# Performance work log

Measured on AMD Instinct MI355X. Metric: run time of the kernel, lower is better.

Reference implementation:

```python
import jax, jax.numpy as jnp
import numpy as np

B, C, H, W = 32, 1024, 32, 32
KC, VC = 1024, 1024  # key_channels must equal H*W; value_channels must equal in_channels


def setup_inputs() -> dict:
    key = jax.random.key(0)
    ks = jax.random.split(key, 8)
    s = 1.0 / np.sqrt(C)
    return {
        "x": jax.random.normal(ks[0], (B, C, H, W), dtype=jnp.float32),
        "Wq": jax.random.normal(ks[1], (KC, C), dtype=jnp.float32) * s,
        "bq": jax.random.normal(ks[2], (KC,), dtype=jnp.float32) * 0.01,
        "Wk": jax.random.normal(ks[3], (KC, C), dtype=jnp.float32) * s,
        "bk": jax.random.normal(ks[4], (KC,), dtype=jnp.float32) * 0.01,
        "Wv": jax.random.normal(ks[5], (VC, C), dtype=jnp.float32) * s,
        "bv": jax.random.normal(ks[6], (VC,), dtype=jnp.float32) * 0.01,
        # torch init is zeros(1); use a nonzero scalar so the attention path is exercised
        "gamma": jax.random.normal(ks[7], (1,), dtype=jnp.float32) * 0.5,
    }


def reference(x, Wq, bq, Wk, bk, Wv, bv, gamma):
    b, c, h, w = x.shape
    n = h * w
    xf = x.reshape(b, c, n)  # [B, C, N]
    # 1x1 convs == per-position channel projections
    q = jnp.einsum('kc,bcn->bkn', Wq, xf) + bq[None, :, None]  # [B, Kc, N]
    k = jnp.einsum('kc,bcn->bkn', Wk, xf) + bk[None, :, None]  # [B, Kc, N]
    v = jnp.einsum('vc,bcn->bvn', Wv, xf) + bv[None, :, None]  # [B, Cv, N]
    # bmm(query, key^T): contracts spatial dim -> channel-channel attention [B, Kc, Kc]
    attn = jax.nn.softmax(jnp.einsum('bin,bjn->bij', q, k), axis=-1)
    # bmm(value, attention): value's spatial dim (== Kc) contracts with attn rows
    out = jnp.einsum('bvn,bnk->bvk', v, attn)  # [B, Cv, Kc] with Kc == N
    out = out.reshape(b, -1, h, w)
    return gamma * out + x
```

## Files before the change

kernel.cpp:

```cpp
#include <hip/hip_runtime.h>
#include <cstdint>

typedef __fp16 f16x8 __attribute__((ext_vector_type(8)));
typedef __fp16 f16x4 __attribute__((ext_vector_type(4)));
typedef float  f32x4 __attribute__((ext_vector_type(4)));

static constexpr int NDIM = 1024;

static constexpr long long OFF_W     = 0;
static constexpr long long OFF_BIAS  = 6291456;
static constexpr long long OFF_XT    = 6303744;
static constexpr long long OFF_S     = 0;
static constexpr long long OFF_QKV   = 134217728;
static constexpr long long OFF_STATS = OFF_QKV + 2097152;

__device__ __forceinline__ void async16(__fp16* lds, const __fp16* g) {
  __builtin_amdgcn_global_load_lds(
      (const __attribute__((address_space(1))) void*)g,
      (__attribute__((address_space(3))) void*)lds, 16, 0, 0);
}

__global__ __launch_bounds__(256) void cast_w(const float* __restrict__ Wq,
                                              const float* __restrict__ Wk,
                                              const float* __restrict__ Wv,
                                              __fp16* __restrict__ W3) {
  const int i = blockIdx.x * 256 + threadIdx.x;
  const int which = i >> 18;
  const int j = i & 262143;
  const float* src = which == 0 ? Wq : (which == 1 ? Wk : Wv);
  const float4 v = ((const float4*)src)[j];
  f16x4 o = {(__fp16)v.x, (__fp16)v.y, (__fp16)v.z, (__fp16)v.w};
  ((f16x4*)W3)[i] = o;
}

__global__ __launch_bounds__(256) void pack_bias(const float* __restrict__ bq,
                                                 const float* __restrict__ bk,
                                                 const float* __restrict__ bv,
                                                 float* __restrict__ b3) {
  const int i = blockIdx.x * 256 + threadIdx.x;
  if (i < 1024) b3[i] = bq[i];
  else if (i < 2048) b3[i] = bk[i - 1024];
  else if (i < 3072) b3[i] = bv[i - 2048];
}

__global__ __launch_bounds__(256) void transpose_cast_x(const float* __restrict__ x,
                                                        __fp16* __restrict__ xT) {
  __shared__ float t[32][33];
  const int b = blockIdx.z;
  const int n0 = blockIdx.x * 32, c0 = blockIdx.y * 32;
  const float* xb = x + (long long)b * NDIM * NDIM;
  __fp16* ob = xT + (long long)b * NDIM * NDIM;
  const int tx = threadIdx.x & 31, ty = threadIdx.x >> 5;
#pragma unroll
  for (int i = ty; i < 32; i += 8)
    t[i][tx] = xb[(long long)(c0 + i) * NDIM + n0 + tx];
  __syncthreads();
#pragma unroll
  for (int i = ty; i < 32; i += 8)
    ob[(long long)(n0 + i) * NDIM + c0 + tx] = (__fp16)t[tx][i];
}


#define STAGE_A(NXT, KN)                                                            \
  async16(&As[(NXT)*8192 + tid*8],        A  + (long long)(m0 + sRow)       * 1024 + (KN) + sCol); \
  async16(&As[(NXT)*8192 + 4096 + tid*8], A  + (long long)(m0 + 128 + sRow) * 1024 + (KN) + sCol);

#define STAGE_B(NXT, KN)                                                            \
  async16(&Bs[(NXT)*8192 + tid*8],        Bp + (long long)(n0 + sRow)       * 1024 + (KN) + sCol); \
  async16(&Bs[(NXT)*8192 + 4096 + tid*8], Bp + (long long)(n0 + 128 + sRow) * 1024 + (KN) + sCol);

#define TILE(BUF, NXT, KN)                                                          \
  asm volatile("s_waitcnt vmcnt(8)" ::: "memory");                                  \
  __builtin_amdgcn_s_barrier();                                                     \
  STAGE_A(NXT, KN)                                                                  \
  STAGE_B(NXT, KN)                                                                  \
  bf[0] = *(const f16x8*)&Bs[(BUF)*8192 + bBase + 0*512];                           \
  bf[1] = *(const f16x8*)&Bs[(BUF)*8192 + bBase + 1*512];                           \
  _Pragma("unroll")                                                                 \
  for (int mf = 0; mf < 8; ++mf)                                                    \
    af[mf] = *(const f16x8*)&As[(BUF)*8192 + aBase + mf*512];                       \
  bf[2] = *(const f16x8*)&Bs[(BUF)*8192 + bBase + 2*512];                           \
  bf[3] = *(const f16x8*)&Bs[(BUF)*8192 + bBase + 3*512];                           \
  _Pragma("unroll")                                                                 \
  for (int mf = 0; mf < 8; ++mf) {                                                  \
    _Pragma("unroll")                                                               \
    for (int nf = 0; nf < 4; ++nf)                                                  \
      acc[mf][nf] = __builtin_amdgcn_mfma_f32_16x16x32_f16(af[mf], bf[nf], acc[mf][nf], 0, 0, 0); \
  }

template <int EPI>
__global__ __launch_bounds__(512, 2)
void gemm256(const __fp16* __restrict__ Ag, const __fp16* __restrict__ Bg,
             void* __restrict__ Cout, const float* __restrict__ bias,
             const float* __restrict__ X, const float* __restrict__ gamma,
             long long sA, long long sB, long long sC) {
  __shared__ alignas(16) __fp16 As[4 * 8192];
  __shared__ alignas(16) __fp16 Bs[4 * 8192];

  const int tid  = threadIdx.x;
  const int wid  = tid >> 6, lane = tid & 63;
  const int wm   = wid >> 2, wn = wid & 3;
  const int g    = lane >> 4, r = lane & 15;
  const int b    = blockIdx.z;
  const int m0   = blockIdx.y * 256;
  const int n0   = blockIdx.x * 256;

  const __fp16* A  = Ag + (long long)b * sA;
  const __fp16* Bp = Bg + (long long)b * sB;

  const int sRow = tid >> 2;
  const int sCol = ((tid & 3) ^ ((tid >> 3) & 3)) * 8;

  const int fcol  = (g ^ ((r >> 1) & 3)) * 8;
  const int aBase = (wm * 128 + r) * 32 + fcol;
  const int bBase = (wn * 64 + r) * 32 + fcol;

  f16x8 af[8];
  f16x8 bf[4];
  f32x4 acc[8][4];
#pragma unroll
  for (int i = 0; i < 8; ++i)
#pragma unroll
    for (int j = 0; j < 4; ++j) acc[i][j] = f32x4{0.f, 0.f, 0.f, 0.f};

  STAGE_A(0, 0)  STAGE_B(0, 0)
  STAGE_A(1, 32) STAGE_B(1, 32)
  STAGE_A(2, 64) STAGE_B(2, 64)

  for (int t0 = 0; t0 < 1024; t0 += 128) {
    const int ka  = t0 + 96;
    const int k0n = (ka < 1024) ? ka : 0;
    const int k1n = (ka + 32 < 1024) ? ka + 32 : 0;
    const int k2n = (ka + 64 < 1024) ? ka + 64 : 0;
    const int k3n = (ka + 96 < 1024) ? ka + 96 : 0;
    TILE(0, 3, k0n)
    TILE(1, 0, k1n)
    TILE(2, 1, k2n)
    TILE(3, 2, k3n)
  }

  const float g2 = (EPI == 2) ? gamma[0] : 0.f;
  const int ccol  = n0 + wn * 64 + r;
  const int crow0 = m0 + wm * 128 + g * 4;
#pragma unroll
  for (int mf = 0; mf < 8; ++mf) {
#pragma unroll
    for (int reg = 0; reg < 4; ++reg) {
      const int row = crow0 + mf * 16 + reg;
      const long long rb = (long long)b * sC + (long long)row * 1024;
      const float bb = (EPI == 0) ? bias[row] : 0.f;
#pragma unroll
      for (int nf = 0; nf < 4; ++nf) {
        const int col = ccol + nf * 16;
        const float v = acc[mf][nf][reg];
        if (EPI == 0)      ((__fp16*)Cout)[rb + col] = (__fp16)(v + bb);
        else if (EPI == 1) ((float*)Cout)[rb + col] = v;
        else               ((float*)Cout)[rb + col] = g2 * v + X[rb + col];
      }
    }
  }
}

__global__ __launch_bounds__(256) void row_stats(const float* __restrict__ S,
                                                 float2* __restrict__ stats) {
  const int row = blockIdx.x * 4 + (threadIdx.x >> 6);
  const int lane = threadIdx.x & 63;
  const float4* rp = (const float4*)(S + (long long)row * NDIM);
  float4 v[4];
  float m = -3.4e38f;
#pragma unroll
  for (int j = 0; j < 4; j++) {
    v[j] = rp[lane + 64 * j];
    m = fmaxf(m, fmaxf(fmaxf(v[j].x, v[j].y), fmaxf(v[j].z, v[j].w)));
  }
#pragma unroll
  for (int o = 32; o; o >>= 1) m = fmaxf(m, __shfl_xor(m, o));
  float s = 0.f;
#pragma unroll
  for (int j = 0; j < 4; j++)
    s += __expf(v[j].x - m) + __expf(v[j].y - m) + __expf(v[j].z - m) + __expf(v[j].w - m);
#pragma unroll
  for (int o = 32; o; o >>= 1) s += __shfl_xor(s, o);
  if (lane == 0) stats[row] = make_float2(m, 1.f / s);
}

__global__ __launch_bounds__(256) void softmax_transpose(const float* __restrict__ S,
                                                         const float2* __restrict__ stats,
                                                         __fp16* __restrict__ attnT) {
  __shared__ __fp16 t[64][72];
  const int b = blockIdx.z;
  const int i0 = blockIdx.y * 64, j0 = blockIdx.x * 64;
  const float* Sb = S + (long long)b * NDIM * NDIM;
  const float2* st = stats + b * NDIM;
  const int tr = threadIdx.x >> 4;
  const int tc = (threadIdx.x & 15) * 4;
#pragma unroll
  for (int it = 0; it < 4; it++) {
    const int i = tr + 16 * it;
    const float4 vv = *(const float4*)&Sb[(long long)(i0 + i) * NDIM + j0 + tc];
    const float2 ms = st[i0 + i];
    t[tc + 0][i] = (__fp16)(__expf(vv.x - ms.x) * ms.y);
    t[tc + 1][i] = (__fp16)(__expf(vv.y - ms.x) * ms.y);
    t[tc + 2][i] = (__fp16)(__expf(vv.z - ms.x) * ms.y);
    t[tc + 3][i] = (__fp16)(__expf(vv.w - ms.x) * ms.y);
  }
  __syncthreads();
  __fp16* Ab = attnT + (long long)b * 3145728;
#pragma unroll
  for (int it = 0; it < 4; it++) {
    const int j = tr + 16 * it;
    f16x4 o = {t[j][tc], t[j][tc + 1], t[j][tc + 2], t[j][tc + 3]};
    *(f16x4*)&Ab[(long long)(j0 + j) * NDIM + i0 + tc] = o;
  }
}

extern "C" void kernel_launch(void* const* d_in, const int* in_sizes, int n_in,
                              void* d_out, int out_size, void* d_ws, size_t ws_size,
                              hipStream_t stream) {
  const float* x     = (const float*)d_in[0];
  const float* Wq    = (const float*)d_in[1];
  const float* bq    = (const float*)d_in[2];
  const float* Wk    = (const float*)d_in[3];
  const float* bk    = (const float*)d_in[4];
  const float* Wv    = (const float*)d_in[5];
  const float* bv    = (const float*)d_in[6];
  const float* gamma = (const float*)d_in[7];
  char* ws = (char*)d_ws;

  __fp16* W3    = (__fp16*)(ws + OFF_W);
  float*  bias3 = (float*)(ws + OFF_BIAS);
  __fp16* xT    = (__fp16*)(ws + OFF_XT);
  float*  S     = (float*)(ws + OFF_S);
  __fp16* QKV   = (__fp16*)(ws + OFF_QKV);
  float2* stats = (float2*)(ws + OFF_STATS);
  float*  out   = (float*)d_out;

  cast_w<<<3072, 256, 0, stream>>>(Wq, Wk, Wv, W3);
  pack_bias<<<12, 256, 0, stream>>>(bq, bk, bv, bias3);
  transpose_cast_x<<<dim3(32, 32, 32), 256, 0, stream>>>(x, xT);

  gemm256<0><<<dim3(4, 12, 32), 512, 0, stream>>>(
      W3, xT, QKV, bias3, nullptr, nullptr,
      0LL, 1048576LL, 3145728LL);

  gemm256<1><<<dim3(4, 4, 32), 512, 0, stream>>>(
      QKV, QKV + 1048576, S, nullptr, nullptr, nullptr,
      3145728LL, 3145728LL, 1048576LL);

  row_stats<<<8192, 256, 0, stream>>>(S, stats);
  softmax_transpose<<<dim3(16, 16, 32), 256, 0, stream>>>(S, stats, QKV);

  gemm256<2><<<dim3(4, 4, 32), 512, 0, stream>>>(
      QKV + 2097152, QKV, out, nullptr, x, gamma,
      3145728LL, 3145728LL, 1048576LL);
}
```

Measured before the change: 532.0 us.

## Fuse softmax row statistics into the QK GEMM epilogue and compute S transposed

The QK GEMM now computes S transposed (K·Qᵀ), so softmax rows become columns. Its epilogue reduces per-column partial max and sum-exp through LDS and writes them to a scratch buffer held in the output tensor. A small finalize kernel merges the four partials, and an elementwise kernel applies exp and normalisation with coalesced reads and writes. This replaces the separate row_stats pass over S and the LDS-transposing softmax kernel, and it also merges the weight-cast and bias-pack launches. The cost is extra epilogue work and reductions inside the GEMM, plus reuse of the output buffer as scratch before the final GEMM overwrites it.

```diff
diff --git a/kernel.cpp b/kernel.cpp
--- a/kernel.cpp
+++ b/kernel.cpp
@@ -12,7 +12,6 @@
 static constexpr long long OFF_XT    = 6303744;
 static constexpr long long OFF_S     = 0;
 static constexpr long long OFF_QKV   = 134217728;
-static constexpr long long OFF_STATS = OFF_QKV + 2097152;
 
 __device__ __forceinline__ void async16(__fp16* lds, const __fp16* g) {
   __builtin_amdgcn_global_load_lds(
@@ -20,27 +19,26 @@
       (__attribute__((address_space(3))) void*)lds, 16, 0, 0);
 }
 
-__global__ __launch_bounds__(256) void cast_w(const float* __restrict__ Wq,
+__global__ __launch_bounds__(256) void prep_w(const float* __restrict__ Wq,
                                               const float* __restrict__ Wk,
                                               const float* __restrict__ Wv,
-                                              __fp16* __restrict__ W3) {
-  const int i = blockIdx.x * 256 + threadIdx.x;
-  const int which = i >> 18;
-  const int j = i & 262143;
-  const float* src = which == 0 ? Wq : (which == 1 ? Wk : Wv);
-  const float4 v = ((const float4*)src)[j];
-  f16x4 o = {(__fp16)v.x, (__fp16)v.y, (__fp16)v.z, (__fp16)v.w};
-  ((f16x4*)W3)[i] = o;
-}
-
-__global__ __launch_bounds__(256) void pack_bias(const float* __restrict__ bq,
-                                                 const float* __restrict__ bk,
-                                                 const float* __restrict__ bv,
-                                                 float* __restrict__ b3) {
-  const int i = blockIdx.x * 256 + threadIdx.x;
-  if (i < 1024) b3[i] = bq[i];
-  else if (i < 2048) b3[i] = bk[i - 1024];
-  else if (i < 3072) b3[i] = bv[i - 2048];
+                                              const float* __restrict__ bq,
+                                              const float* __restrict__ bk,
+                                              const float* __restrict__ bv,
+                                              __fp16* __restrict__ W3,
+                                              float* __restrict__ b3) {
+  if (blockIdx.x < 3072) {
+    const int i = blockIdx.x * 256 + threadIdx.x;
+    const int which = i >> 18;
+    const int j = i & 262143;
+    const float* src = which == 0 ? Wq : (which == 1 ? Wk : Wv);
+    const float4 v = ((const float4*)src)[j];
+    f16x4 o = {(__fp16)v.x, (__fp16)v.y, (__fp16)v.z, (__fp16)v.w};
+    ((f16x4*)W3)[i] = o;
+  } else {
+    for (int k = threadIdx.x; k < 3072; k += 256)
+      b3[k] = (k < 1024) ? bq[k] : (k < 2048) ? bk[k - 1024] : bv[k - 2048];
+  }
 }
 
 __global__ __launch_bounds__(256) void transpose_cast_x(const float* __restrict__ x,
@@ -93,6 +91,7 @@
 void gemm256(const __fp16* __restrict__ Ag, const __fp16* __restrict__ Bg,
              void* __restrict__ Cout, const float* __restrict__ bias,
              const float* __restrict__ X, const float* __restrict__ gamma,
+             float2* __restrict__ part,
              long long sA, long long sB, long long sC) {
   __shared__ alignas(16) __fp16 As[4 * 8192];
   __shared__ alignas(16) __fp16 Bs[4 * 8192];
@@ -142,6 +141,39 @@
   const float g2 = (EPI == 2) ? gamma[0] : 0.f;
   const int ccol  = n0 + wn * 64 + r;
   const int crow0 = m0 + wm * 128 + g * 4;
+
+  if (EPI == 1) {
+    asm volatile("s_waitcnt vmcnt(0)" ::: "memory");
+    __syncthreads();
+    float2* LDSp = (float2*)As;
+#pragma unroll
+    for (int nf = 0; nf < 4; ++nf) {
+      float pm = -3.4e38f;
+#pragma unroll
+      for (int mf = 0; mf < 8; ++mf)
+#pragma unroll
+        for (int rg = 0; rg < 4; ++rg) pm = fmaxf(pm, acc[mf][nf][rg]);
+      pm = fmaxf(pm, __shfl_xor(pm, 16));
+      pm = fmaxf(pm, __shfl_xor(pm, 32));
+      float ps = 0.f;
+#pragma unroll
+      for (int mf = 0; mf < 8; ++mf)
+#pragma unroll
+        for (int rg = 0; rg < 4; ++rg) ps += __expf(acc[mf][nf][rg] - pm);
+      ps += __shfl_xor(ps, 16);
+      ps += __shfl_xor(ps, 32);
+      if (lane < 16)
+        LDSp[(wn * 64 + nf * 16 + r) * 2 + wm] = make_float2(pm, ps);
+    }
+    __syncthreads();
+    if (tid < 256) {
+      const float2 a = LDSp[tid * 2 + 0], c2 = LDSp[tid * 2 + 1];
+      const float M = fmaxf(a.x, c2.x);
+      const float Sv = a.y * __expf(a.x - M) + c2.y * __expf(c2.x - M);
+      part[(long long)blockIdx.y * 32768 + b * 1024 + n0 + tid] = make_float2(M, Sv);
+    }
+  }
+
 #pragma unroll
   for (int mf = 0; mf < 8; ++mf) {
 #pragma unroll
@@ -161,56 +193,45 @@
   }
 }
 
-__global__ __launch_bounds__(256) void row_stats(const float* __restrict__ S,
-                                                 float2* __restrict__ stats) {
-  const int row = blockIdx.x * 4 + (threadIdx.x >> 6);
-  const int lane = threadIdx.x & 63;
-  const float4* rp = (const float4*)(S + (long long)row * NDIM);
-  float4 v[4];
-  float m = -3.4e38f;
-#pragma unroll
-  for (int j = 0; j < 4; j++) {
-    v[j] = rp[lane + 64 * j];
-    m = fmaxf(m, fmaxf(fmaxf(v[j].x, v[j].y), fmaxf(v[j].z, v[j].w)));
-  }
-#pragma unroll
-  for (int o = 32; o; o >>= 1) m = fmaxf(m, __shfl_xor(m, o));
-  float s = 0.f;
-#pragma unroll
-  for (int j = 0; j < 4; j++)
-    s += __expf(v[j].x - m) + __expf(v[j].y - m) + __expf(v[j].z - m) + __expf(v[j].w - m);
-#pragma unroll
-  for (int o = 32; o; o >>= 1) s += __shfl_xor(s, o);
-  if (lane == 0) stats[row] = make_float2(m, 1.f / s);
-}
-
-__global__ __launch_bounds__(256) void softmax_transpose(const float* __restrict__ S,
-                                                         const float2* __restrict__ stats,
-                                                         __fp16* __restrict__ attnT) {
-  __shared__ __fp16 t[64][72];
-  const int b = blockIdx.z;
-  const int i0 = blockIdx.y * 64, j0 = blockIdx.x * 64;
-  const float* Sb = S + (long long)b * NDIM * NDIM;
-  const float2* st = stats + b * NDIM;
-  const int tr = threadIdx.x >> 4;
-  const int tc = (threadIdx.x & 15) * 4;
-#pragma unroll
-  for (int it = 0; it < 4; it++) {
-    const int i = tr + 16 * it;
-    const float4 vv = *(const float4*)&Sb[(long long)(i0 + i) * NDIM + j0 + tc];
-    const float2 ms = st[i0 + i];
-    t[tc + 0][i] = (__fp16)(__expf(vv.x - ms.x) * ms.y);
-    t[tc + 1][i] = (__fp16)(__expf(vv.y - ms.x) * ms.y);
-    t[tc + 2][i] = (__fp16)(__expf(vv.z - ms.x) * ms.y);
-    t[tc + 3][i] = (__fp16)(__expf(vv.w - ms.x) * ms.y);
-  }
-  __syncthreads();
-  __fp16* Ab = attnT + (long long)b * 3145728;
-#pragma unroll
-  for (int it = 0; it < 4; it++) {
-    const int j = tr + 16 * it;
-    f16x4 o = {t[j][tc], t[j][tc + 1], t[j][tc + 2], t[j][tc + 3]};
-    *(f16x4*)&Ab[(long long)(j0 + j) * NDIM + i0 + tc] = o;
+__global__ __launch_bounds__(256) void finalize_stats(const float2* __restrict__ part,
+                                                      float2* __restrict__ stats) {
+  const int i = blockIdx.x * 256 + threadIdx.x;
+  float2 p0 = part[i];
+  float2 p1 = part[32768 + i];
+  float2 p2 = part[65536 + i];
+  float2 p3 = part[98304 + i];
+  float M = fmaxf(fmaxf(p0.x, p1.x), fmaxf(p2.x, p3.x));
+  float S = p0.y * __expf(p0.x - M) + p1.y * __expf(p1.x - M) +
+            p2.y * __expf(p2.x - M) + p3.y * __expf(p3.x - M);
+  stats[i] = make_float2(M, 1.f / S);
+}
+
+__global__ __launch_bounds__(256) void softmax_elem(const float* __restrict__ St,
+                                                    const float2* __restrict__ stats,
+                                                    __fp16* __restrict__ attnT) {
+  const long long idx0 = ((long long)blockIdx.x * 256 + threadIdx.x) * 16;
+  const int b   = (int)(idx0 >> 20);
+  const int rem = (int)(idx0 & 1048575);
+  const int n0  = rem & 1023;
+  const float4* src = (const float4*)(St + idx0);
+  const float2* st  = stats + b * 1024 + n0;
+  __fp16* dst = attnT + (long long)b * 3145728 + rem;
+  float w[16];
+#pragma unroll
+  for (int j = 0; j < 4; ++j) {
+    const float4 v = src[j];
+    const float2 s0 = st[j * 4 + 0], s1 = st[j * 4 + 1], s2 = st[j * 4 + 2], s3 = st[j * 4 + 3];
+    w[j * 4 + 0] = __expf(v.x - s0.x) * s0.y;
+    w[j * 4 + 1] = __expf(v.y - s1.x) * s1.y;
+    w[j * 4 + 2] = __expf(v.z - s2.x) * s2.y;
+    w[j * 4 + 3] = __expf(v.w - s3.x) * s3.y;
+  }
+#pragma unroll
+  for (int h = 0; h < 2; ++h) {
+    f16x8 o;
+#pragma unroll
+    for (int e = 0; e < 8; ++e) o[e] = (__fp16)w[h * 8 + e];
+    *(f16x8*)(dst + h * 8) = o;
   }
 }
 
@@ -230,27 +251,27 @@
   __fp16* W3    = (__fp16*)(ws + OFF_W);
   float*  bias3 = (float*)(ws + OFF_BIAS);
   __fp16* xT    = (__fp16*)(ws + OFF_XT);
-  float*  S     = (float*)(ws + OFF_S);
+  float*  St    = (float*)(ws + OFF_S);
   __fp16* QKV   = (__fp16*)(ws + OFF_QKV);
-  float2* stats = (float2*)(ws + OFF_STATS);
   float*  out   = (float*)d_out;
-
-  cast_w<<<3072, 256, 0, stream>>>(Wq, Wk, Wv, W3);
-  pack_bias<<<12, 256, 0, stream>>>(bq, bk, bv, bias3);
+  float2* part  = (float2*)d_out;
+  float2* stats = (float2*)d_out + 131072;
+
+  prep_w<<<3073, 256, 0, stream>>>(Wq, Wk, Wv, bq, bk, bv, W3, bias3);
   transpose_cast_x<<<dim3(32, 32, 32), 256, 0, stream>>>(x, xT);
 
   gemm256<0><<<dim3(4, 12, 32), 512, 0, stream>>>(
-      W3, xT, QKV, bias3, nullptr, nullptr,
+      W3, xT, QKV, bias3, nullptr, nullptr, nullptr,
       0LL, 1048576LL, 3145728LL);
 
   gemm256<1><<<dim3(4, 4, 32), 512, 0, stream>>>(
-      QKV, QKV + 1048576, S, nullptr, nullptr, nullptr,
+      QKV + 1048576, QKV, St, nullptr, nullptr, nullptr, part,
       3145728LL, 3145728LL, 1048576LL);
 
-  row_stats<<<8192, 256, 0, stream>>>(S, stats);
-  softmax_transpose<<<dim3(16, 16, 32), 256, 0, stream>>>(S, stats, QKV);
+  finalize_stats<<<128, 256, 0, stream>>>(part, stats);
+  softmax_elem<<<8192, 256, 0, stream>>>(St, stats, QKV);
 
   gemm256<2><<<dim3(4, 4, 32), 512, 0, stream>>>(
-      QKV + 2097152, QKV, out, nullptr, x, gamma,
+      QKV + 2097152, QKV, out, nullptr, x, gamma, nullptr,
       3145728LL, 3145728LL, 1048576LL);
 }
```

After: 544.8 us. 2.4% more time.

## Fuse softmax row statistics into QK^T GEMM epilogue and merge prep kernels

Applied to the files above, without the earlier changes.

The QK^T GEMM epilogue now computes per-row partial max and sum-of-exp over each 256-column tile. It reduces them across waves through LDS and writes the partials to a scratch area inside the output buffer. A small finalize kernel merges the four partials per row, replacing the row_stats kernel that re-read the whole 128MB score matrix. The weight cast and bias pack are also merged into one launch. This trades a full pass over S for extra epilogue work and reuses the output buffer as temporary storage, which the final GEMM later overwrites.

```diff
diff --git a/kernel.cpp b/kernel.cpp
--- a/kernel.cpp
+++ b/kernel.cpp
@@ -12,7 +12,6 @@
 static constexpr long long OFF_XT    = 6303744;
 static constexpr long long OFF_S     = 0;
 static constexpr long long OFF_QKV   = 134217728;
-static constexpr long long OFF_STATS = OFF_QKV + 2097152;
 
 __device__ __forceinline__ void async16(__fp16* lds, const __fp16* g) {
   __builtin_amdgcn_global_load_lds(
@@ -20,27 +19,26 @@
       (__attribute__((address_space(3))) void*)lds, 16, 0, 0);
 }
 
-__global__ __launch_bounds__(256) void cast_w(const float* __restrict__ Wq,
+__global__ __launch_bounds__(256) void prep_w(const float* __restrict__ Wq,
                                               const float* __restrict__ Wk,
                                               const float* __restrict__ Wv,
-                                              __fp16* __restrict__ W3) {
-  const int i = blockIdx.x * 256 + threadIdx.x;
-  const int which = i >> 18;
-  const int j = i & 262143;
-  const float* src = which == 0 ? Wq : (which == 1 ? Wk : Wv);
-  const float4 v = ((const float4*)src)[j];
-  f16x4 o = {(__fp16)v.x, (__fp16)v.y, (__fp16)v.z, (__fp16)v.w};
-  ((f16x4*)W3)[i] = o;
-}
-
-__global__ __launch_bounds__(256) void pack_bias(const float* __restrict__ bq,
-                                                 const float* __restrict__ bk,
-                                                 const float* __restrict__ bv,
-                                                 float* __restrict__ b3) {
-  const int i = blockIdx.x * 256 + threadIdx.x;
-  if (i < 1024) b3[i] = bq[i];
-  else if (i < 2048) b3[i] = bk[i - 1024];
-  else if (i < 3072) b3[i] = bv[i - 2048];
+                                              const float* __restrict__ bq,
+                                              const float* __restrict__ bk,
+                                              const float* __restrict__ bv,
+                                              __fp16* __restrict__ W3,
+                                              float* __restrict__ b3) {
+  if (blockIdx.x < 3072) {
+    const int i = blockIdx.x * 256 + threadIdx.x;
+    const int which = i >> 18;
+    const int j = i & 262143;
+    const float* src = which == 0 ? Wq : (which == 1 ? Wk : Wv);
+    const float4 v = ((const float4*)src)[j];
+    f16x4 o = {(__fp16)v.x, (__fp16)v.y, (__fp16)v.z, (__fp16)v.w};
+    ((f16x4*)W3)[i] = o;
+  } else {
+    for (int k = threadIdx.x; k < 3072; k += 256)
+      b3[k] = (k < 1024) ? bq[k] : (k < 2048) ? bk[k - 1024] : bv[k - 2048];
+  }
 }
 
 __global__ __launch_bounds__(256) void transpose_cast_x(const float* __restrict__ x,
@@ -93,6 +91,7 @@
 void gemm256(const __fp16* __restrict__ Ag, const __fp16* __restrict__ Bg,
              void* __restrict__ Cout, const float* __restrict__ bias,
              const float* __restrict__ X, const float* __restrict__ gamma,
+             float2* __restrict__ part,
              long long sA, long long sB, long long sC) {
   __shared__ alignas(16) __fp16 As[4 * 8192];
   __shared__ alignas(16) __fp16 Bs[4 * 8192];
@@ -142,6 +141,44 @@
   const float g2 = (EPI == 2) ? gamma[0] : 0.f;
   const int ccol  = n0 + wn * 64 + r;
   const int crow0 = m0 + wm * 128 + g * 4;
+
+  if (EPI == 1) {
+    asm volatile("s_waitcnt vmcnt(0)" ::: "memory");
+    __syncthreads();
+    float2* LDSp = (float2*)As;
+#pragma unroll
+    for (int mf = 0; mf < 8; ++mf) {
+#pragma unroll
+      for (int reg = 0; reg < 4; ++reg) {
+        float M = fmaxf(fmaxf(acc[mf][0][reg], acc[mf][1][reg]),
+                        fmaxf(acc[mf][2][reg], acc[mf][3][reg]));
+        M = fmaxf(M, __shfl_xor(M, 1));
+        M = fmaxf(M, __shfl_xor(M, 2));
+        M = fmaxf(M, __shfl_xor(M, 4));
+        M = fmaxf(M, __shfl_xor(M, 8));
+        float Sv = __expf(acc[mf][0][reg] - M) + __expf(acc[mf][1][reg] - M) +
+                   __expf(acc[mf][2][reg] - M) + __expf(acc[mf][3][reg] - M);
+        Sv += __shfl_xor(Sv, 1);
+        Sv += __shfl_xor(Sv, 2);
+        Sv += __shfl_xor(Sv, 4);
+        Sv += __shfl_xor(Sv, 8);
+        if (r == 0) {
+          const int rl = wm * 128 + mf * 16 + g * 4 + reg;
+          LDSp[rl * 4 + wn] = make_float2(M, Sv);
+        }
+      }
+    }
+    __syncthreads();
+    if (tid < 256) {
+      const float2 p0 = LDSp[tid * 4 + 0], p1 = LDSp[tid * 4 + 1];
+      const float2 p2 = LDSp[tid * 4 + 2], p3 = LDSp[tid * 4 + 3];
+      const float M = fmaxf(fmaxf(p0.x, p1.x), fmaxf(p2.x, p3.x));
+      const float Sv = p0.y * __expf(p0.x - M) + p1.y * __expf(p1.x - M) +
+                       p2.y * __expf(p2.x - M) + p3.y * __expf(p3.x - M);
+      part[(long long)blockIdx.x * 32768 + b * 1024 + m0 + tid] = make_float2(M, Sv);
+    }
+  }
+
 #pragma unroll
   for (int mf = 0; mf < 8; ++mf) {
 #pragma unroll
@@ -161,27 +198,17 @@
   }
 }
 
-__global__ __launch_bounds__(256) void row_stats(const float* __restrict__ S,
-                                                 float2* __restrict__ stats) {
-  const int row = blockIdx.x * 4 + (threadIdx.x >> 6);
-  const int lane = threadIdx.x & 63;
-  const float4* rp = (const float4*)(S + (long long)row * NDIM);
-  float4 v[4];
-  float m = -3.4e38f;
-#pragma unroll
-  for (int j = 0; j < 4; j++) {
-    v[j] = rp[lane + 64 * j];
-    m = fmaxf(m, fmaxf(fmaxf(v[j].x, v[j].y), fmaxf(v[j].z, v[j].w)));
-  }
-#pragma unroll
-  for (int o = 32; o; o >>= 1) m = fmaxf(m, __shfl_xor(m, o));
-  float s = 0.f;
-#pragma unroll
-  for (int j = 0; j < 4; j++)
-    s += __expf(v[j].x - m) + __expf(v[j].y - m) + __expf(v[j].z - m) + __expf(v[j].w - m);
-#pragma unroll
-  for (int o = 32; o; o >>= 1) s += __shfl_xor(s, o);
-  if (lane == 0) stats[row] = make_float2(m, 1.f / s);
+__global__ __launch_bounds__(256) void finalize_stats(const float2* __restrict__ part,
+                                                      float2* __restrict__ stats) {
+  const int i = blockIdx.x * 256 + threadIdx.x;
+  float2 p0 = part[i];
+  float2 p1 = part[32768 + i];
+  float2 p2 = part[65536 + i];
+  float2 p3 = part[98304 + i];
+  float M = fmaxf(fmaxf(p0.x, p1.x), fmaxf(p2.x, p3.x));
+  float S = p0.y * __expf(p0.x - M) + p1.y * __expf(p1.x - M) +
+            p2.y * __expf(p2.x - M) + p3.y * __expf(p3.x - M);
+  stats[i] = make_float2(M, 1.f / S);
 }
 
 __global__ __launch_bounds__(256) void softmax_transpose(const float* __restrict__ S,
@@ -232,25 +259,25 @@
   __fp16* xT    = (__fp16*)(ws + OFF_XT);
   float*  S     = (float*)(ws + OFF_S);
   __fp16* QKV   = (__fp16*)(ws + OFF_QKV);
-  float2* stats = (float2*)(ws + OFF_STATS);
   float*  out   = (float*)d_out;
-
-  cast_w<<<3072, 256, 0, stream>>>(Wq, Wk, Wv, W3);
-  pack_bias<<<12, 256, 0, stream>>>(bq, bk, bv, bias3);
+  float2* part  = (float2*)d_out;
+  float2* stats = (float2*)d_out + 131072;
+
+  prep_w<<<3073, 256, 0, stream>>>(Wq, Wk, Wv, bq, bk, bv, W3, bias3);
   transpose_cast_x<<<dim3(32, 32, 32), 256, 0, stream>>>(x, xT);
 
   gemm256<0><<<dim3(4, 12, 32), 512, 0, stream>>>(
-      W3, xT, QKV, bias3, nullptr, nullptr,
+      W3, xT, QKV, bias3, nullptr, nullptr, nullptr,
       0LL, 1048576LL, 3145728LL);
 
   gemm256<1><<<dim3(4, 4, 32), 512, 0, stream>>>(
-      QKV, QKV + 1048576, S, nullptr, nullptr, nullptr,
+      QKV, QKV + 1048576, S, nullptr, nullptr, nullptr, part,
       3145728LL, 3145728LL, 1048576LL);
 
-  row_stats<<<8192, 256, 0, stream>>>(S, stats);
+  finalize_stats<<<128, 256, 0, stream>>>(part, stats);
   softmax_transpose<<<dim3(16, 16, 32), 256, 0, stream>>>(S, stats, QKV);
 
   gemm256<2><<<dim3(4, 4, 32), 512, 0, stream>>>(
-      QKV + 2097152, QKV, out, nullptr, x, gamma,
+      QKV + 2097152, QKV, out, nullptr, x, gamma, nullptr,
       3145728LL, 3145728LL, 1048576LL);
 }
```

New measurement: 537.2 us. About the same (+1.0%).
